# Optimization experiments

Hardware: AMD Instinct MI355X
Metric: run time of the kernel (lower is better)

## Reference

```python
import jax, jax.numpy as jnp
import numpy as np
import math

N_CLASSES = 1000
CODE_LENGTH = 1024
IN_FEATURES = 4096
BATCH = 512
MAX_PROB = 0.95
POWER = 1.0


def _hadamard(n):
    # Sylvester construction; n must be a power of 2.
    H = np.array([[1.0]], dtype=np.float64)
    while H.shape[0] < n:
        H = np.block([[H, H], [H, -H]])
    return H


def setup_inputs() -> dict:
    key = jax.random.key(0)
    k1, k2, k3 = jax.random.split(key, 3)
    x = jax.random.normal(k1, (BATCH, IN_FEATURES), dtype=jnp.float32)
    out_feat = CODE_LENGTH - 1  # single head: code_length//1 - 1
    # nn.Linear default init: U(-1/sqrt(fan_in), 1/sqrt(fan_in))
    bound = 1.0 / math.sqrt(IN_FEATURES)
    W = jax.random.uniform(k2, (out_feat, IN_FEATURES), dtype=jnp.float32, minval=-bound, maxval=bound)
    b = jax.random.uniform(k3, (out_feat,), dtype=jnp.float32, minval=-bound, maxval=bound)
    labels = jnp.asarray(_hadamard(CODE_LENGTH)[:N_CLASSES, 1:], dtype=jnp.float32)  # (C, L-1)
    eps = jnp.float32(CODE_LENGTH * math.pow((1.0 - MAX_PROB) / (MAX_PROB * (N_CLASSES - 1)), 1.0 / POWER))
    power = jnp.float32(POWER)
    return {"x": x, "W": W, "b": b, "labels": labels, "eps": eps, "power": power}


def reference(x, W, b, labels, eps, power):
    # Linear head: (B, in) @ (in, L-1) + b
    h = jnp.tanh(x @ W.T + b)                               # (B, L-1)
    # L1 distance to each Hadamard code row: (B, 1, L-1) vs (C, L-1)
    d = jnp.sum(jnp.abs(h[:, None, :] - labels), axis=-1)   # (B, C)
    d = jnp.maximum(d, eps)
    inv = 1.0 / jnp.power(d, power)                          # (B, C)
    return inv / jnp.sum(inv, axis=-1, keepdims=True)
```

## Files before the change

### kernel.cpp

```cpp
#include <hip/hip_runtime.h>

#define BATCH 512
#define INFEAT 4096
#define LOUT 1023
#define NCLS 1000
#define NPAD 1024
#define SPLITK 4

typedef __bf16 bf16x8 __attribute__((ext_vector_type(8)));
typedef float f32x4 __attribute__((ext_vector_type(4)));

__device__ __forceinline__ unsigned f2bf2(float a, float b) {
    unsigned ua = __builtin_bit_cast(unsigned, a);
    unsigned ub = __builtin_bit_cast(unsigned, b);
    ua = (ua + 0x7fffu + ((ua >> 16) & 1u)) >> 16;
    ub = (ub + 0x7fffu + ((ub >> 16) & 1u)) >> 16;
    return ua | (ub << 16);
}

__device__ __forceinline__ void gload_lds16(const void* g, void* l) {
    __builtin_amdgcn_global_load_lds(
        (const __attribute__((address_space(1))) void*)g,
        (__attribute__((address_space(3))) void*)l, 16, 0, 0);
}

__global__ __launch_bounds__(256) void k_cvt(const float* __restrict__ x,
                                             const float* __restrict__ W,
                                             unsigned char* __restrict__ xb,
                                             unsigned char* __restrict__ Wb) {
    int blk = blockIdx.x;
    if (blk < 1024) {
        int g = blk * 256 + threadIdx.x;
        int r = g >> 9, k16 = g & 511;
        const float4* p = (const float4*)(x + (size_t)r * INFEAT + k16 * 8);
        float4 v0 = p[0], v1 = p[1];
        uint4 o;
        o.x = f2bf2(v0.x, v0.y); o.y = f2bf2(v0.z, v0.w);
        o.z = f2bf2(v1.x, v1.y); o.w = f2bf2(v1.z, v1.w);
        *(uint4*)(xb + (size_t)r * 8192 + (k16 >> 3) * 128 + (((k16 & 7) ^ (r & 7)) * 16)) = o;
    } else {
        int g = (blk - 1024) * 256 + threadIdx.x;
        int r = g >> 9, k16 = g & 511;
        uint4 o = {0, 0, 0, 0};
        if (r < LOUT) {
            const float4* p = (const float4*)(W + (size_t)r * INFEAT + k16 * 8);
            float4 v0 = p[0], v1 = p[1];
            o.x = f2bf2(v0.x, v0.y); o.y = f2bf2(v0.z, v0.w);
            o.z = f2bf2(v1.x, v1.y); o.w = f2bf2(v1.z, v1.w);
        }
        *(uint4*)(Wb + (size_t)r * 8192 + (k16 >> 3) * 128 + (((k16 & 7) ^ (r & 7)) * 16)) = o;
    }
}

__global__ __launch_bounds__(256, 2) void k_gemm1(
    const unsigned char* __restrict__ xb, const unsigned char* __restrict__ Wb,
    float* __restrict__ partial) {
    __shared__ unsigned char lds[32768];
    f32x4 acc[2][2] = {};
    const int bn = blockIdx.x, bm = blockIdx.y, sp = blockIdx.z;
    const int tid = threadIdx.x;
    const int wave = tid >> 6, lane = tid & 63;
    const int lrow = lane & 15, lgrp = lane >> 4;
    const int wr = wave >> 1, wc = wave & 1;
    const int arow0 = bm * 64, brow0 = bn * 64, chunk0 = sp * 16;

    auto STAGE = [&](int bsel, int c) {
        unsigned char* lA = lds + bsel * 16384;
        unsigned char* lB = lA + 8192;
#pragma unroll
        for (int rr = 0; rr < 2; ++rr) {
            int g = rr * 256 + tid;
            int r = g >> 3, s = g & 7;
            gload_lds16(xb + (size_t)(arow0 + r) * 8192 + c * 128 + s * 16,
                        lA + (rr * 256 + wave * 64) * 16);
            gload_lds16(Wb + (size_t)(brow0 + r) * 8192 + c * 128 + s * 16,
                        lB + (rr * 256 + wave * 64) * 16);
        }
    };

    auto COMPUTE = [&](int bsel) {
        const unsigned char* lA = lds + bsel * 16384;
        const unsigned char* lB = lA + 8192;
#pragma unroll
        for (int ks = 0; ks < 2; ++ks) {
            int swz = ((ks * 4 + lgrp) ^ (lrow & 7)) * 16;
            bf16x8 a[2], b[2];
#pragma unroll
            for (int m = 0; m < 2; ++m)
                a[m] = *(const bf16x8*)(lA + (wr * 32 + m * 16 + lrow) * 128 + swz);
#pragma unroll
            for (int n = 0; n < 2; ++n)
                b[n] = *(const bf16x8*)(lB + (wc * 32 + n * 16 + lrow) * 128 + swz);
#pragma unroll
            for (int m = 0; m < 2; ++m)
#pragma unroll
                for (int n = 0; n < 2; ++n)
                    acc[m][n] = __builtin_amdgcn_mfma_f32_16x16x32_bf16(
                        a[m], b[n], acc[m][n], 0, 0, 0);
        }
    };

    STAGE(0, chunk0);
    asm volatile("s_waitcnt vmcnt(0)" ::: "memory");
    __syncthreads();
#pragma unroll 1
    for (int t = 0; t < 16; ++t) {
        int cur = t & 1;
        if (t + 1 < 16) STAGE(cur ^ 1, chunk0 + t + 1);
        COMPUTE(cur);
        asm volatile("s_waitcnt vmcnt(0)" ::: "memory");
        __syncthreads();
    }

    float* P = partial + (size_t)sp * (BATCH * NPAD);
#pragma unroll
    for (int m = 0; m < 2; ++m)
#pragma unroll
        for (int n = 0; n < 2; ++n)
#pragma unroll
            for (int reg = 0; reg < 4; ++reg) {
                int r = arow0 + wr * 32 + m * 16 + lgrp * 4 + reg;
                int c = brow0 + wc * 32 + n * 16 + lrow;
                P[(size_t)r * NPAD + c] = acc[m][n][reg];
            }
}

__global__ __launch_bounds__(256) void k_fused(const float* __restrict__ partial,
                                               const float* __restrict__ bias,
                                               const float* __restrict__ epsp,
                                               const float* __restrict__ powp,
                                               float* __restrict__ out) {
    __shared__ float g[1024];
    __shared__ float wsum[4];
    const int r = blockIdx.x, t = threadIdx.x;
    const int n0 = t * 4;

    f32x4 v = {0.0f, 0.0f, 0.0f, 0.0f};
#pragma unroll
    for (int s = 0; s < SPLITK; ++s) {
        float4 p = *(const float4*)(partial + ((size_t)s * BATCH + r) * NPAD + n0);
        v[0] += p.x; v[1] += p.y; v[2] += p.z; v[3] += p.w;
    }
    float bb[4];
    if (t < 255) {
        float4 b4 = *(const float4*)(bias + n0);
        bb[0] = b4.x; bb[1] = b4.y; bb[2] = b4.z; bb[3] = b4.w;
    } else {
        bb[0] = bias[1020]; bb[1] = bias[1021]; bb[2] = bias[1022]; bb[3] = 0.0f;
    }
    if (t == 0) g[0] = 0.0f;
#pragma unroll
    for (int j = 0; j < 4; ++j) {
        int n = n0 + j;
        if (n < LOUT) g[n + 1] = tanhf(v[j] + bb[j]);
    }
    __syncthreads();

#pragma unroll 1
    for (int s = 0; s < 10; ++s) {
        int st = 1 << s;
#pragma unroll
        for (int pp = 0; pp < 2; ++pp) {
            int p = t + pp * 256;
            int idx = ((p >> s) << (s + 1)) | (p & (st - 1));
            float a = g[idx], c = g[idx + st];
            g[idx] = a + c;
            g[idx + st] = a - c;
        }
        __syncthreads();
    }

    const float eps = *epsp, pw = *powp;
    float iv[4];
    float ss = 0.0f;
#pragma unroll
    for (int j = 0; j < 4; ++j) {
        int c = n0 + j;
        float d = fmaxf(1023.0f - g[c], eps);
        float q = (pw == 1.0f) ? (1.0f / d) : powf(d, -pw);
        if (c >= NCLS) q = 0.0f;
        iv[j] = q;
        ss += q;
    }
#pragma unroll
    for (int m = 32; m; m >>= 1) ss += __shfl_xor(ss, m, 64);
    if ((t & 63) == 0) wsum[t >> 6] = ss;
    __syncthreads();
    float sc = 1.0f / (wsum[0] + wsum[1] + wsum[2] + wsum[3]);

    if (n0 < NCLS) {
        float4 o;
        o.x = iv[0] * sc; o.y = iv[1] * sc; o.z = iv[2] * sc; o.w = iv[3] * sc;
        *(float4*)(out + (size_t)r * NCLS + n0) = o;
    }
}

extern "C" void kernel_launch(void* const* d_in, const int* in_sizes, int n_in,
                              void* d_out, int out_size, void* d_ws, size_t ws_size,
                              hipStream_t stream) {
    const float* x = (const float*)d_in[0];
    const float* W = (const float*)d_in[1];
    const float* b = (const float*)d_in[2];
    const float* epsp = (const float*)d_in[4];
    const float* powp = (const float*)d_in[5];
    float* out = (float*)d_out;

    unsigned char* ws = (unsigned char*)d_ws;
    unsigned char* xb = ws;
    unsigned char* Wb = ws + (4u << 20);
    float* partial = (float*)(ws + (12u << 20));

    k_cvt<<<3072, 256, 0, stream>>>(x, W, xb, Wb);
    k_gemm1<<<dim3(16, 8, 4), 256, 0, stream>>>(xb, Wb, partial);
    k_fused<<<512, 256, 0, stream>>>(partial, b, epsp, powp, out);
}
```

Baseline: 29.38 us.

## Enlarge GEMM M-tile to 128, double split-K, store partials as bf16

The GEMM block tile grows from 64x64 to 128x64, with four M fragments per wave, so each loaded W tile is reused across more rows. Split-K doubles from 4 to 8, which keeps the grid at 512 blocks while halving the K loop per block. Partial sums are now written as bf16 instead of fp32 to cut the traffic of writing and re-reading partials in the fused epilogue. In exchange, the bf16 partials add rounding error before tanh, LDS use per block rises to 48KB, and accumulator register pressure grows.

```diff
diff --git a/kernel.cpp b/kernel.cpp
--- a/kernel.cpp
+++ b/kernel.cpp
@@ -5,17 +5,20 @@
 #define LOUT 1023
 #define NCLS 1000
 #define NPAD 1024
-#define SPLITK 4
+#define SPLITK 8
 
 typedef __bf16 bf16x8 __attribute__((ext_vector_type(8)));
 typedef float f32x4 __attribute__((ext_vector_type(4)));
 
+__device__ __forceinline__ unsigned short f2bf(float a) {
+    unsigned u = __builtin_bit_cast(unsigned, a);
+    return (unsigned short)((u + 0x7fffu + ((u >> 16) & 1u)) >> 16);
+}
 __device__ __forceinline__ unsigned f2bf2(float a, float b) {
-    unsigned ua = __builtin_bit_cast(unsigned, a);
-    unsigned ub = __builtin_bit_cast(unsigned, b);
-    ua = (ua + 0x7fffu + ((ua >> 16) & 1u)) >> 16;
-    ub = (ub + 0x7fffu + ((ub >> 16) & 1u)) >> 16;
-    return ua | (ub << 16);
+    return (unsigned)f2bf(a) | ((unsigned)f2bf(b) << 16);
+}
+__device__ __forceinline__ float bf2f(unsigned short u) {
+    return __builtin_bit_cast(float, ((unsigned)u) << 16);
 }
 
 __device__ __forceinline__ void gload_lds16(const void* g, void* l) {
@@ -54,45 +57,50 @@
 
 __global__ __launch_bounds__(256, 2) void k_gemm1(
     const unsigned char* __restrict__ xb, const unsigned char* __restrict__ Wb,
-    float* __restrict__ partial) {
-    __shared__ unsigned char lds[32768];
-    f32x4 acc[2][2] = {};
+    unsigned short* __restrict__ partial) {
+    __shared__ unsigned char lds[49152];
+    f32x4 acc[4][2] = {};
     const int bn = blockIdx.x, bm = blockIdx.y, sp = blockIdx.z;
     const int tid = threadIdx.x;
     const int wave = tid >> 6, lane = tid & 63;
     const int lrow = lane & 15, lgrp = lane >> 4;
     const int wr = wave >> 1, wc = wave & 1;
-    const int arow0 = bm * 64, brow0 = bn * 64, chunk0 = sp * 16;
+    const int arow0 = bm * 128, brow0 = bn * 64, chunk0 = sp * 8;
 
     auto STAGE = [&](int bsel, int c) {
-        unsigned char* lA = lds + bsel * 16384;
-        unsigned char* lB = lA + 8192;
-#pragma unroll
-        for (int rr = 0; rr < 2; ++rr) {
+        unsigned char* lA = lds + bsel * 24576;
+        unsigned char* lB = lA + 16384;
+#pragma unroll
+        for (int rr = 0; rr < 4; ++rr) {
             int g = rr * 256 + tid;
             int r = g >> 3, s = g & 7;
             gload_lds16(xb + (size_t)(arow0 + r) * 8192 + c * 128 + s * 16,
                         lA + (rr * 256 + wave * 64) * 16);
+        }
+#pragma unroll
+        for (int rr = 0; rr < 2; ++rr) {
+            int g = rr * 256 + tid;
+            int r = g >> 3, s = g & 7;
             gload_lds16(Wb + (size_t)(brow0 + r) * 8192 + c * 128 + s * 16,
                         lB + (rr * 256 + wave * 64) * 16);
         }
     };
 
     auto COMPUTE = [&](int bsel) {
-        const unsigned char* lA = lds + bsel * 16384;
-        const unsigned char* lB = lA + 8192;
+        const unsigned char* lA = lds + bsel * 24576;
+        const unsigned char* lB = lA + 16384;
 #pragma unroll
         for (int ks = 0; ks < 2; ++ks) {
             int swz = ((ks * 4 + lgrp) ^ (lrow & 7)) * 16;
-            bf16x8 a[2], b[2];
-#pragma unroll
-            for (int m = 0; m < 2; ++m)
-                a[m] = *(const bf16x8*)(lA + (wr * 32 + m * 16 + lrow) * 128 + swz);
+            bf16x8 a[4], b[2];
+#pragma unroll
+            for (int m = 0; m < 4; ++m)
+                a[m] = *(const bf16x8*)(lA + (wr * 64 + m * 16 + lrow) * 128 + swz);
 #pragma unroll
             for (int n = 0; n < 2; ++n)
                 b[n] = *(const bf16x8*)(lB + (wc * 32 + n * 16 + lrow) * 128 + swz);
 #pragma unroll
-            for (int m = 0; m < 2; ++m)
+            for (int m = 0; m < 4; ++m)
 #pragma unroll
                 for (int n = 0; n < 2; ++n)
                     acc[m][n] = __builtin_amdgcn_mfma_f32_16x16x32_bf16(
@@ -104,28 +112,28 @@
     asm volatile("s_waitcnt vmcnt(0)" ::: "memory");
     __syncthreads();
 #pragma unroll 1
-    for (int t = 0; t < 16; ++t) {
+    for (int t = 0; t < 8; ++t) {
         int cur = t & 1;
-        if (t + 1 < 16) STAGE(cur ^ 1, chunk0 + t + 1);
+        if (t + 1 < 8) STAGE(cur ^ 1, chunk0 + t + 1);
         COMPUTE(cur);
         asm volatile("s_waitcnt vmcnt(0)" ::: "memory");
         __syncthreads();
     }
 
-    float* P = partial + (size_t)sp * (BATCH * NPAD);
-#pragma unroll
-    for (int m = 0; m < 2; ++m)
+    unsigned short* P = partial + (size_t)sp * (BATCH * NPAD);
+#pragma unroll
+    for (int m = 0; m < 4; ++m)
 #pragma unroll
         for (int n = 0; n < 2; ++n)
 #pragma unroll
             for (int reg = 0; reg < 4; ++reg) {
-                int r = arow0 + wr * 32 + m * 16 + lgrp * 4 + reg;
+                int r = arow0 + wr * 64 + m * 16 + lgrp * 4 + reg;
                 int c = brow0 + wc * 32 + n * 16 + lrow;
-                P[(size_t)r * NPAD + c] = acc[m][n][reg];
+                P[(size_t)r * NPAD + c] = f2bf(acc[m][n][reg]);
             }
 }
 
-__global__ __launch_bounds__(256) void k_fused(const float* __restrict__ partial,
+__global__ __launch_bounds__(256) void k_fused(const unsigned short* __restrict__ partial,
                                                const float* __restrict__ bias,
                                                const float* __restrict__ epsp,
                                                const float* __restrict__ powp,
@@ -138,8 +146,8 @@
     f32x4 v = {0.0f, 0.0f, 0.0f, 0.0f};
 #pragma unroll
     for (int s = 0; s < SPLITK; ++s) {
-        float4 p = *(const float4*)(partial + ((size_t)s * BATCH + r) * NPAD + n0);
-        v[0] += p.x; v[1] += p.y; v[2] += p.z; v[3] += p.w;
+        ushort4 p = *(const ushort4*)(partial + ((size_t)s * BATCH + r) * NPAD + n0);
+        v[0] += bf2f(p.x); v[1] += bf2f(p.y); v[2] += bf2f(p.z); v[3] += bf2f(p.w);
     }
     float bb[4];
     if (t < 255) {
@@ -208,9 +216,9 @@
     unsigned char* ws = (unsigned char*)d_ws;
     unsigned char* xb = ws;
     unsigned char* Wb = ws + (4u << 20);
-    float* partial = (float*)(ws + (12u << 20));
+    unsigned short* partial = (unsigned short*)(ws + (12u << 20));
 
     k_cvt<<<3072, 256, 0, stream>>>(x, W, xb, Wb);
-    k_gemm1<<<dim3(16, 8, 4), 256, 0, stream>>>(xb, Wb, partial);
+    k_gemm1<<<dim3(16, 4, 8), 256, 0, stream>>>(xb, Wb, partial);
     k_fused<<<512, 256, 0, stream>>>(partial, b, epsp, powp, out);
 }
```

Result: faster. 27.93 us (-4.9%).
